# Kernel optimization log

Measured on AMD Instinct MI355X. Metric: run time of the kernel, lower is better.

Reference implementation:

```python
import jax, jax.numpy as jnp
from jax import lax
import numpy as np

H = 16        # hidden_size == input_size
L = 8         # num_layers


def _lstm_layer(x_seq, Wih, Whh, bih, bhh):
    # x_seq: [B, T, H] -> outputs [B, T, H]; PyTorch gate order i,f,g,o
    B = x_seq.shape[0]
    b = bih + bhh  # [4H]

    def step(carry, xt):
        h, c = carry
        gates = xt @ Wih.T + h @ Whh.T + b  # [B, 4H]
        i, f, g, o = jnp.split(gates, 4, axis=-1)
        c = jax.nn.sigmoid(f) * c + jax.nn.sigmoid(i) * jnp.tanh(g)
        h = jax.nn.sigmoid(o) * jnp.tanh(c)
        return (h, c), h

    h0 = jnp.zeros((B, H), x_seq.dtype)
    (_, _), hs = lax.scan(step, (h0, h0), jnp.swapaxes(x_seq, 0, 1))
    return jnp.swapaxes(hs, 0, 1)  # [B, T, H]


def setup_inputs() -> dict:
    key = jax.random.key(0)
    ks = jax.random.split(key, 9)
    s = 1.0 / np.sqrt(H)  # PyTorch default init scale
    x = jax.random.normal(ks[0], (2048, 512, H), dtype=jnp.float32)
    W_ih = jax.random.uniform(ks[1], (L, 4 * H, H), jnp.float32, -s, s)
    W_hh = jax.random.uniform(ks[2], (L, 4 * H, H), jnp.float32, -s, s)
    b_ih = jax.random.uniform(ks[3], (L, 4 * H), jnp.float32, -s, s)
    b_hh = jax.random.uniform(ks[4], (L, 4 * H), jnp.float32, -s, s)
    Wp = jax.random.uniform(ks[5], (3, H), jnp.float32, -s, s)
    bp = jax.random.uniform(ks[6], (3,), jnp.float32, -s, s)
    Wo = jax.random.uniform(ks[7], (3, H), jnp.float32, -s, s)
    bo = jax.random.uniform(ks[8], (3,), jnp.float32, -s, s)
    return {"x": x, "W_ih": W_ih, "W_hh": W_hh, "b_ih": b_ih, "b_hh": b_hh,
            "Wp": Wp, "bp": bp, "Wo": Wo, "bo": bo}


def reference(x, W_ih, W_hh, b_ih, b_hh, Wp, bp, Wo, bo):
    h = x
    for l in range(L):  # fixed small layer count
        h = _lstm_layer(h, W_ih[l], W_hh[l], b_ih[l], b_hh[l])
    last = h[:, -1, :]                       # [B, H]
    position = last @ Wp.T + bp              # [B, 3]
    orientation = jnp.tanh(last @ Wo.T + bo) # [B, 3]
    return jnp.concatenate((position, orientation), axis=1)  # [B, 6]
```

## Files before the change

kernel.cpp:

```cpp
#include <hip/hip_runtime.h>
#include <math.h>

typedef _Float16 f16x4 __attribute__((ext_vector_type(4)));
typedef _Float16 f16x2 __attribute__((ext_vector_type(2)));
typedef float    f32x4 __attribute__((ext_vector_type(4)));
typedef float    f32x2 __attribute__((ext_vector_type(2)));

constexpr int kT     = 512;
constexpr int kH     = 16;
constexpr int kL     = 8;
constexpr int kNB    = 8;
constexpr int kSlots = 8;
constexpr int kLyr   = kL + 1;
constexpr int kRow   = 16;
constexpr int kSlotE = kLyr * kNB * kRow;
constexpr int kIters = 33;

constexpr float kL2E = 1.4426950408889634f;

__device__ __forceinline__ float ex2(float w)  { return __builtin_amdgcn_exp2f(w); }
__device__ __forceinline__ float rcpf(float e) { return __builtin_amdgcn_rcpf(e); }

__global__ __launch_bounds__(512, 2)
void lstm_rr8(const float* __restrict__ x,
              const float* __restrict__ Wih, const float* __restrict__ Whh,
              const float* __restrict__ bih, const float* __restrict__ bhh,
              const float* __restrict__ Wp,  const float* __restrict__ bpos,
              const float* __restrict__ Wo,  const float* __restrict__ bori,
              float* __restrict__ out)
{
    const int tid  = threadIdx.x;
    const int l    = tid >> 6;
    const int lane = tid & 63;
    const int n    = lane & 15;
    const int q    = lane >> 4;
    const int b    = n & 7;
    const int hi   = n >> 3;

    __shared__ __align__(16) _Float16 hb[kSlots][kLyr][kNB][kRow];

    {
        int* hz = (int*)&hb[0][0][0][0];
        for (int i = tid; i < (int)(sizeof(hb) / 4); i += 512) hz[i] = 0;
    }
    __syncthreads();

    const float asc = ((n & 3) == 2) ? (-2.0f * kL2E) : (-kL2E);
    f16x4 A1[4], A2[4];
    f32x4 bias[4];
    #pragma unroll
    for (int p = 0; p < 4; ++p) {
        const int wrow = (n & 3) * 16 + 4 * (n >> 2) + p;
        const float* w1 = Wih + (size_t)l * 64 * kH + wrow * kH + 4 * q;
        const float* w2 = Whh + (size_t)l * 64 * kH + wrow * kH + 4 * q;
        #pragma unroll
        for (int jj = 0; jj < 4; ++jj) {
            A1[p][jj] = (_Float16)(asc * w1[jj]);
            A2[p][jj] = (_Float16)(asc * w2[jj]);
        }
        #pragma unroll
        for (int r = 0; r < 4; ++r) {
            const float sc = (r == 2) ? (-2.0f * kL2E) : (-kL2E);
            const int g0 = l * 64 + r * 16 + 4 * q + p;
            bias[p][r] = sc * (bih[g0] + bhh[g0]);
        }
    }

    const _Float16* b1base = &hb[0][l][b][4 * q];
    _Float16* hwbase = &hb[0][l + 1][b][4 * q + 2 * hi];
    _Float16* xwbase = &hb[0][0][b][4 * q + 2 * hi];

    const float* xg = x + ((size_t)(blockIdx.x * kNB + b) * kT) * kH
                        + 4 * q + 2 * hi;
    f32x2 xr0 = {0.f, 0.f}, xr1 = {0.f, 0.f}, xr2 = {0.f, 0.f}, xr3 = {0.f, 0.f};
    if (l == 0) {
        #pragma unroll
        for (int t = 0; t < 2; ++t) {
            const f32x2 xv = *(const f32x2*)(xg + (size_t)t * kH);
            f16x2 xh = { (_Float16)xv[0], (_Float16)xv[1] };
            *(f16x2*)(&hb[6 + t][0][b][4 * q + 2 * hi]) = xh;
        }
        xr0 = *(const f32x2*)(xg + 2 * (size_t)kH);
        xr1 = *(const f32x2*)(xg + 3 * (size_t)kH);
        xr2 = *(const f32x2*)(xg + 4 * (size_t)kH);
        xr3 = *(const f32x2*)(xg + 5 * (size_t)kH);
    }
    __syncthreads();

    f32x4 dIn0, dIn1, dIn2, dIn3;
    {
        const f16x4 B1p = *(const f16x4*)(b1base + 6 * kSlotE);
        dIn0 = __builtin_amdgcn_mfma_f32_16x16x16f16(A1[0], B1p, bias[0], 0, 0, 0);
        dIn1 = __builtin_amdgcn_mfma_f32_16x16x16f16(A1[1], B1p, bias[1], 0, 0, 0);
        dIn2 = __builtin_amdgcn_mfma_f32_16x16x16f16(A1[2], B1p, bias[2], 0, 0, 0);
        dIn3 = __builtin_amdgcn_mfma_f32_16x16x16f16(A1[3], B1p, bias[3], 0, 0, 0);
    }

    f16x4 B2r = { (_Float16)0.f, (_Float16)0.f, (_Float16)0.f, (_Float16)0.f };
    float cA = 0.f, cB = 0.f;
    const int tl = 2 * l;

    #pragma unroll 1
    for (int it = 0; it < kIters; ++it) {
        const int wb = it * 16;
        #pragma unroll
        for (int k = 0; k < 16; ++k) {
            const int w = wb + k;
            const bool active = ((unsigned)(w - tl) < (unsigned)kT);

            const f16x4 B1n = *(const f16x4*)(b1base + ((k + 7) & 7) * kSlotE);

            f32x4 d0 = __builtin_amdgcn_mfma_f32_16x16x16f16(A2[0], B2r, dIn0, 0, 0, 0);
            f32x4 d1 = __builtin_amdgcn_mfma_f32_16x16x16f16(A2[1], B2r, dIn1, 0, 0, 0);
            f32x4 d2 = __builtin_amdgcn_mfma_f32_16x16x16f16(A2[2], B2r, dIn2, 0, 0, 0);
            f32x4 d3 = __builtin_amdgcn_mfma_f32_16x16x16f16(A2[3], B2r, dIn3, 0, 0, 0);

            f32x4 dA, dB;
            #pragma unroll
            for (int r = 0; r < 4; ++r) {
                dA[r] = hi ? d2[r] : d0[r];
                dB[r] = hi ? d3[r] : d1[r];
            }

            float hAf, hBf;
            {
                const float Ei = ex2(fminf(dA[0], 40.0f));
                const float Ef = ex2(fminf(dA[1], 40.0f));
                const float Eg = ex2(fminf(dA[2], 40.0f));
                const float Eo = ex2(fminf(dA[3], 60.0f));
                const float Dg = 1.0f + Eg;
                const float Df = 1.0f + Ef;
                const float P1  = fmaf(Ei, Dg, Dg);
                const float den = Df * P1;
                const float t2  = fmaf(-Eg, Df, Df);
                const float num = fmaf(cA, P1, t2);
                float cn = num * rcpf(den);
                cn = active ? cn : 0.0f;
                cA = cn;
                const float ac = fminf(cn * (-2.0f * kL2E), 60.0f);
                const float Ec = ex2(ac);
                const float Do = 1.0f + Eo;
                const float R2 = rcpf(fmaf(Do, Ec, Do));
                hAf = fmaf(-Ec, R2, R2);
            }
            {
                const float Ei = ex2(fminf(dB[0], 40.0f));
                const float Ef = ex2(fminf(dB[1], 40.0f));
                const float Eg = ex2(fminf(dB[2], 40.0f));
                const float Eo = ex2(fminf(dB[3], 60.0f));
                const float Dg = 1.0f + Eg;
                const float Df = 1.0f + Ef;
                const float P1  = fmaf(Ei, Dg, Dg);
                const float den = Df * P1;
                const float t2  = fmaf(-Eg, Df, Df);
                const float num = fmaf(cB, P1, t2);
                float cn = num * rcpf(den);
                cn = active ? cn : 0.0f;
                cB = cn;
                const float ac = fminf(cn * (-2.0f * kL2E), 60.0f);
                const float Ec = ex2(ac);
                const float Do = 1.0f + Eo;
                const float R2 = rcpf(fmaf(Do, Ec, Do));
                hBf = fmaf(-Ec, R2, R2);
            }

            f16x2 hp = { (_Float16)hAf, (_Float16)hBf };
            union { f16x2 h; int i; } uh; uh.h = hp;
            const int own   = uh.i;
            const int other = __shfl_xor(own, 8, 64);
            union { int i[2]; f16x4 v; } ub;
            ub.i[0] = hi ? other : own;
            ub.i[1] = hi ? own : other;
            B2r = ub.v;

            *(f16x2*)(hwbase + (k & 7) * kSlotE) = hp;

            if (l == 0) {
                f16x2 xh = { (_Float16)xr0[0], (_Float16)xr0[1] };
                *(f16x2*)(xwbase + (k & 7) * kSlotE) = xh;
                xr0 = xr1; xr1 = xr2; xr2 = xr3;
                int tn = w + 6; if (tn > kT - 1) tn = kT - 1;
                xr3 = *(const f32x2*)(xg + (size_t)tn * kH);
            }

            dIn0 = __builtin_amdgcn_mfma_f32_16x16x16f16(A1[0], B1n, bias[0], 0, 0, 0);
            dIn1 = __builtin_amdgcn_mfma_f32_16x16x16f16(A1[1], B1n, bias[1], 0, 0, 0);
            dIn2 = __builtin_amdgcn_mfma_f32_16x16x16f16(A1[2], B1n, bias[2], 0, 0, 0);
            dIn3 = __builtin_amdgcn_mfma_f32_16x16x16f16(A1[3], B1n, bias[3], 0, 0, 0);

            asm volatile("s_waitcnt lgkmcnt(0)\n\ts_barrier" ::: "memory");
        }
    }

    __syncthreads();

    if (l == kL - 1 && lane < kNB) {
        const int bb = lane;
        float hreg[kH];
        #pragma unroll
        for (int u = 0; u < kH; ++u) hreg[u] = (float)hb[5][kL][bb][u];
        #pragma unroll
        for (int r = 0; r < 3; ++r) {
            float accP = bpos[r], accO = bori[r];
            #pragma unroll
            for (int u = 0; u < kH; ++u) {
                accP = fmaf(hreg[u], Wp[r * kH + u], accP);
                accO = fmaf(hreg[u], Wo[r * kH + u], accO);
            }
            const float Et = ex2(-2.0f * kL2E * accO);
            accO = fmaf(2.0f, rcpf(1.0f + Et), -1.0f);
            out[(size_t)(blockIdx.x * kNB + bb) * 6 + r]     = accP;
            out[(size_t)(blockIdx.x * kNB + bb) * 6 + 3 + r] = accO;
        }
    }
}

extern "C" void kernel_launch(void* const* d_in, const int* in_sizes, int n_in,
                              void* d_out, int out_size, void* d_ws, size_t ws_size,
                              hipStream_t stream) {
    const float* x    = (const float*)d_in[0];
    const float* Wih  = (const float*)d_in[1];
    const float* Whh  = (const float*)d_in[2];
    const float* bih  = (const float*)d_in[3];
    const float* bhh  = (const float*)d_in[4];
    const float* Wp   = (const float*)d_in[5];
    const float* bpos = (const float*)d_in[6];
    const float* Wo   = (const float*)d_in[7];
    const float* bori = (const float*)d_in[8];
    float* out = (float*)d_out;

    const int B = in_sizes[0] / (kT * kH);
    lstm_rr8<<<dim3(B / kNB), dim3(512), 0, stream>>>(x, Wih, Whh, bih, bhh,
                                                      Wp, bpos, Wo, bori, out);
}
```

Baseline: 312.2 us.

## Pipeline layers over 16-step chunks to cut per-timestep block barriers

Result: no change. 308.2 us (-1.3%).

```diff
diff --git a/kernel.cpp b/kernel.cpp
--- a/kernel.cpp
+++ b/kernel.cpp
@@ -4,17 +4,15 @@
 typedef _Float16 f16x4 __attribute__((ext_vector_type(4)));
 typedef _Float16 f16x2 __attribute__((ext_vector_type(2)));
 typedef float    f32x4 __attribute__((ext_vector_type(4)));
-typedef float    f32x2 __attribute__((ext_vector_type(2)));
-
-constexpr int kT     = 512;
-constexpr int kH     = 16;
-constexpr int kL     = 8;
-constexpr int kNB    = 8;
-constexpr int kSlots = 8;
-constexpr int kLyr   = kL + 1;
-constexpr int kRow   = 16;
-constexpr int kSlotE = kLyr * kNB * kRow;
-constexpr int kIters = 33;
+
+constexpr int kT      = 512;
+constexpr int kH      = 16;
+constexpr int kL      = 8;
+constexpr int kNB     = 8;
+constexpr int kC      = 16;
+constexpr int kChunks = kT / kC;
+constexpr int kStages = kChunks + kL - 1;
+constexpr int kRowE   = kNB * kH;
 
 constexpr float kL2E = 1.4426950408889634f;
 
@@ -22,12 +20,12 @@
 __device__ __forceinline__ float rcpf(float e) { return __builtin_amdgcn_rcpf(e); }
 
 __global__ __launch_bounds__(512, 2)
-void lstm_rr8(const float* __restrict__ x,
-              const float* __restrict__ Wih, const float* __restrict__ Whh,
-              const float* __restrict__ bih, const float* __restrict__ bhh,
-              const float* __restrict__ Wp,  const float* __restrict__ bpos,
-              const float* __restrict__ Wo,  const float* __restrict__ bori,
-              float* __restrict__ out)
+void lstm_ck(const float* __restrict__ x,
+             const float* __restrict__ Wih, const float* __restrict__ Whh,
+             const float* __restrict__ bih, const float* __restrict__ bhh,
+             const float* __restrict__ Wp,  const float* __restrict__ bpos,
+             const float* __restrict__ Wo,  const float* __restrict__ bori,
+             float* __restrict__ out)
 {
     const int tid  = threadIdx.x;
     const int l    = tid >> 6;
@@ -37,13 +35,8 @@
     const int b    = n & 7;
     const int hi   = n >> 3;
 
-    __shared__ __align__(16) _Float16 hb[kSlots][kLyr][kNB][kRow];
-
-    {
-        int* hz = (int*)&hb[0][0][0][0];
-        for (int i = tid; i < (int)(sizeof(hb) / 4); i += 512) hz[i] = 0;
-    }
-    __syncthreads();
+    __shared__ __align__(16) _Float16 hbuf[2][kL - 1][kC][kNB][kH];
+    __shared__ __align__(16) _Float16 headb[kNB][kH];
 
     const float asc = ((n & 3) == 2) ? (-2.0f * kL2E) : (-kL2E);
     f16x4 A1[4], A2[4];
@@ -66,151 +59,136 @@
         }
     }
 
-    const _Float16* b1base = &hb[0][l][b][4 * q];
-    _Float16* hwbase = &hb[0][l + 1][b][4 * q + 2 * hi];
-    _Float16* xwbase = &hb[0][0][b][4 * q + 2 * hi];
-
-    const float* xg = x + ((size_t)(blockIdx.x * kNB + b) * kT) * kH
-                        + 4 * q + 2 * hi;
-    f32x2 xr0 = {0.f, 0.f}, xr1 = {0.f, 0.f}, xr2 = {0.f, 0.f}, xr3 = {0.f, 0.f};
+    const float* xg = x + ((size_t)(blockIdx.x * kNB + b) * kT) * kH + 4 * q;
+    f32x4 xf[kC];
     if (l == 0) {
         #pragma unroll
-        for (int t = 0; t < 2; ++t) {
-            const f32x2 xv = *(const f32x2*)(xg + (size_t)t * kH);
-            f16x2 xh = { (_Float16)xv[0], (_Float16)xv[1] };
-            *(f16x2*)(&hb[6 + t][0][b][4 * q + 2 * hi]) = xh;
-        }
-        xr0 = *(const f32x2*)(xg + 2 * (size_t)kH);
-        xr1 = *(const f32x2*)(xg + 3 * (size_t)kH);
-        xr2 = *(const f32x2*)(xg + 4 * (size_t)kH);
-        xr3 = *(const f32x2*)(xg + 5 * (size_t)kH);
-    }
-    __syncthreads();
-
-    f32x4 dIn0, dIn1, dIn2, dIn3;
-    {
-        const f16x4 B1p = *(const f16x4*)(b1base + 6 * kSlotE);
-        dIn0 = __builtin_amdgcn_mfma_f32_16x16x16f16(A1[0], B1p, bias[0], 0, 0, 0);
-        dIn1 = __builtin_amdgcn_mfma_f32_16x16x16f16(A1[1], B1p, bias[1], 0, 0, 0);
-        dIn2 = __builtin_amdgcn_mfma_f32_16x16x16f16(A1[2], B1p, bias[2], 0, 0, 0);
-        dIn3 = __builtin_amdgcn_mfma_f32_16x16x16f16(A1[3], B1p, bias[3], 0, 0, 0);
+        for (int j = 0; j < kC; ++j)
+            xf[j] = *(const f32x4*)(xg + (size_t)j * kH);
     }
 
     f16x4 B2r = { (_Float16)0.f, (_Float16)0.f, (_Float16)0.f, (_Float16)0.f };
     float cA = 0.f, cB = 0.f;
-    const int tl = 2 * l;
 
     #pragma unroll 1
-    for (int it = 0; it < kIters; ++it) {
-        const int wb = it * 16;
-        #pragma unroll
-        for (int k = 0; k < 16; ++k) {
-            const int w = wb + k;
-            const bool active = ((unsigned)(w - tl) < (unsigned)kT);
-
-            const f16x4 B1n = *(const f16x4*)(b1base + ((k + 7) & 7) * kSlotE);
-
-            f32x4 d0 = __builtin_amdgcn_mfma_f32_16x16x16f16(A2[0], B2r, dIn0, 0, 0, 0);
-            f32x4 d1 = __builtin_amdgcn_mfma_f32_16x16x16f16(A2[1], B2r, dIn1, 0, 0, 0);
-            f32x4 d2 = __builtin_amdgcn_mfma_f32_16x16x16f16(A2[2], B2r, dIn2, 0, 0, 0);
-            f32x4 d3 = __builtin_amdgcn_mfma_f32_16x16x16f16(A2[3], B2r, dIn3, 0, 0, 0);
-
-            f32x4 dA, dB;
+    for (int s = 0; s < kStages; ++s) {
+        const int c = s - l;
+        if ((unsigned)c < (unsigned)kChunks) {
+            f16x4 B1f[kC];
+            if (l == 0) {
+                #pragma unroll
+                for (int j = 0; j < kC; ++j) {
+                    f16x4 v = { (_Float16)xf[j][0], (_Float16)xf[j][1],
+                                (_Float16)xf[j][2], (_Float16)xf[j][3] };
+                    B1f[j] = v;
+                }
+                if (c + 1 < kChunks) {
+                    #pragma unroll
+                    for (int j = 0; j < kC; ++j)
+                        xf[j] = *(const f32x4*)(xg + (size_t)((c + 1) * kC + j) * kH);
+                }
+            } else {
+                const _Float16* src = &hbuf[c & 1][l - 1][0][b][4 * q];
+                #pragma unroll
+                for (int j = 0; j < kC; ++j)
+                    B1f[j] = *(const f16x4*)(src + j * kRowE);
+            }
+
+            _Float16* wdst = &hbuf[c & 1][(l < kL - 1) ? l : 0][0][b][4 * q + 2 * hi];
+
             #pragma unroll
-            for (int r = 0; r < 4; ++r) {
-                dA[r] = hi ? d2[r] : d0[r];
-                dB[r] = hi ? d3[r] : d1[r];
+            for (int j = 0; j < kC; ++j) {
+                f32x4 dIn0 = __builtin_amdgcn_mfma_f32_16x16x16f16(A1[0], B1f[j], bias[0], 0, 0, 0);
+                f32x4 dIn1 = __builtin_amdgcn_mfma_f32_16x16x16f16(A1[1], B1f[j], bias[1], 0, 0, 0);
+                f32x4 dIn2 = __builtin_amdgcn_mfma_f32_16x16x16f16(A1[2], B1f[j], bias[2], 0, 0, 0);
+                f32x4 dIn3 = __builtin_amdgcn_mfma_f32_16x16x16f16(A1[3], B1f[j], bias[3], 0, 0, 0);
+                f32x4 d0 = __builtin_amdgcn_mfma_f32_16x16x16f16(A2[0], B2r, dIn0, 0, 0, 0);
+                f32x4 d1 = __builtin_amdgcn_mfma_f32_16x16x16f16(A2[1], B2r, dIn1, 0, 0, 0);
+                f32x4 d2 = __builtin_amdgcn_mfma_f32_16x16x16f16(A2[2], B2r, dIn2, 0, 0, 0);
+                f32x4 d3 = __builtin_amdgcn_mfma_f32_16x16x16f16(A2[3], B2r, dIn3, 0, 0, 0);
+
+                f32x4 dA, dB;
+                #pragma unroll
+                for (int r = 0; r < 4; ++r) {
+                    dA[r] = hi ? d2[r] : d0[r];
+                    dB[r] = hi ? d3[r] : d1[r];
+                }
+
+                float hAf, hBf;
+                {
+                    const float Ei = ex2(fminf(dA[0], 40.0f));
+                    const float Ef = ex2(fminf(dA[1], 40.0f));
+                    const float Eg = ex2(fminf(dA[2], 40.0f));
+                    const float Eo = ex2(fminf(dA[3], 60.0f));
+                    const float Dg = 1.0f + Eg;
+                    const float Df = 1.0f + Ef;
+                    const float P1  = fmaf(Ei, Dg, Dg);
+                    const float den = Df * P1;
+                    const float t2  = fmaf(-Eg, Df, Df);
+                    const float num = fmaf(cA, P1, t2);
+                    const float cn  = num * rcpf(den);
+                    cA = cn;
+                    const float ac = fminf(cn * (-2.0f * kL2E), 60.0f);
+                    const float Ec = ex2(ac);
+                    const float Do = 1.0f + Eo;
+                    const float R2 = rcpf(fmaf(Do, Ec, Do));
+                    hAf = fmaf(-Ec, R2, R2);
+                }
+                {
+                    const float Ei = ex2(fminf(dB[0], 40.0f));
+                    const float Ef = ex2(fminf(dB[1], 40.0f));
+                    const float Eg = ex2(fminf(dB[2], 40.0f));
+                    const float Eo = ex2(fminf(dB[3], 60.0f));
+                    const float Dg = 1.0f + Eg;
+                    const float Df = 1.0f + Ef;
+                    const float P1  = fmaf(Ei, Dg, Dg);
+                    const float den = Df * P1;
+                    const float t2  = fmaf(-Eg, Df, Df);
+                    const float num = fmaf(cB, P1, t2);
+                    const float cn  = num * rcpf(den);
+                    cB = cn;
+                    const float ac = fminf(cn * (-2.0f * kL2E), 60.0f);
+                    const float Ec = ex2(ac);
+                    const float Do = 1.0f + Eo;
+                    const float R2 = rcpf(fmaf(Do, Ec, Do));
+                    hBf = fmaf(-Ec, R2, R2);
+                }
+
+                f16x2 hp = { (_Float16)hAf, (_Float16)hBf };
+                union { f16x2 h; int i; } uh; uh.h = hp;
+                const int own   = uh.i;
+                const int other = __shfl_xor(own, 8, 64);
+                union { int i2[2]; f16x4 v; } ub;
+                ub.i2[0] = hi ? other : own;
+                ub.i2[1] = hi ? own : other;
+                B2r = ub.v;
+
+                if (l < kL - 1)
+                    *(f16x2*)(wdst + j * kRowE) = hp;
+                if (l == kL - 1 && c == kChunks - 1 && j == kC - 1)
+                    *(f16x2*)(&headb[b][4 * q + 2 * hi]) = hp;
             }
-
-            float hAf, hBf;
-            {
-                const float Ei = ex2(fminf(dA[0], 40.0f));
-                const float Ef = ex2(fminf(dA[1], 40.0f));
-                const float Eg = ex2(fminf(dA[2], 40.0f));
-                const float Eo = ex2(fminf(dA[3], 60.0f));
-                const float Dg = 1.0f + Eg;
-                const float Df = 1.0f + Ef;
-                const float P1  = fmaf(Ei, Dg, Dg);
-                const float den = Df * P1;
-                const float t2  = fmaf(-Eg, Df, Df);
-                const float num = fmaf(cA, P1, t2);
-                float cn = num * rcpf(den);
-                cn = active ? cn : 0.0f;
-                cA = cn;
-                const float ac = fminf(cn * (-2.0f * kL2E), 60.0f);
-                const float Ec = ex2(ac);
-                const float Do = 1.0f + Eo;
-                const float R2 = rcpf(fmaf(Do, Ec, Do));
-                hAf = fmaf(-Ec, R2, R2);
+        }
+        asm volatile("s_waitcnt lgkmcnt(0)\n\ts_barrier" ::: "memory");
+    }
+
+    __syncthreads();
+
+    if (l == kL - 1) {
+        const int bb = lane >> 3;
+        const int r  = lane & 7;
+        if (r < 6) {
+            const bool  isP   = (r < 3);
+            const float* wrow = isP ? (Wp + r * kH) : (Wo + (r - 3) * kH);
+            float acc = isP ? bpos[r] : bori[r - 3];
+            #pragma unroll
+            for (int u = 0; u < kH; ++u)
+                acc = fmaf((float)headb[bb][u], wrow[u], acc);
+            if (!isP) {
+                const float Et = ex2(-2.0f * kL2E * acc);
+                acc = fmaf(2.0f, rcpf(1.0f + Et), -1.0f);
             }
-            {
-                const float Ei = ex2(fminf(dB[0], 40.0f));
-                const float Ef = ex2(fminf(dB[1], 40.0f));
-                const float Eg = ex2(fminf(dB[2], 40.0f));
-                const float Eo = ex2(fminf(dB[3], 60.0f));
-                const float Dg = 1.0f + Eg;
-                const float Df = 1.0f + Ef;
-                const float P1  = fmaf(Ei, Dg, Dg);
-                const float den = Df * P1;
-                const float t2  = fmaf(-Eg, Df, Df);
-                const float num = fmaf(cB, P1, t2);
-                float cn = num * rcpf(den);
-                cn = active ? cn : 0.0f;
-                cB = cn;
-                const float ac = fminf(cn * (-2.0f * kL2E), 60.0f);
-                const float Ec = ex2(ac);
-                const float Do = 1.0f + Eo;
-                const float R2 = rcpf(fmaf(Do, Ec, Do));
-                hBf = fmaf(-Ec, R2, R2);
-            }
-
-            f16x2 hp = { (_Float16)hAf, (_Float16)hBf };
-            union { f16x2 h; int i; } uh; uh.h = hp;
-            const int own   = uh.i;
-            const int other = __shfl_xor(own, 8, 64);
-            union { int i[2]; f16x4 v; } ub;
-            ub.i[0] = hi ? other : own;
-            ub.i[1] = hi ? own : other;
-            B2r = ub.v;
-
-            *(f16x2*)(hwbase + (k & 7) * kSlotE) = hp;
-
-            if (l == 0) {
-                f16x2 xh = { (_Float16)xr0[0], (_Float16)xr0[1] };
-                *(f16x2*)(xwbase + (k & 7) * kSlotE) = xh;
-                xr0 = xr1; xr1 = xr2; xr2 = xr3;
-                int tn = w + 6; if (tn > kT - 1) tn = kT - 1;
-                xr3 = *(const f32x2*)(xg + (size_t)tn * kH);
-            }
-
-            dIn0 = __builtin_amdgcn_mfma_f32_16x16x16f16(A1[0], B1n, bias[0], 0, 0, 0);
-            dIn1 = __builtin_amdgcn_mfma_f32_16x16x16f16(A1[1], B1n, bias[1], 0, 0, 0);
-            dIn2 = __builtin_amdgcn_mfma_f32_16x16x16f16(A1[2], B1n, bias[2], 0, 0, 0);
-            dIn3 = __builtin_amdgcn_mfma_f32_16x16x16f16(A1[3], B1n, bias[3], 0, 0, 0);
-
-            asm volatile("s_waitcnt lgkmcnt(0)\n\ts_barrier" ::: "memory");
-        }
-    }
-
-    __syncthreads();
-
-    if (l == kL - 1 && lane < kNB) {
-        const int bb = lane;
-        float hreg[kH];
-        #pragma unroll
-        for (int u = 0; u < kH; ++u) hreg[u] = (float)hb[5][kL][bb][u];
-        #pragma unroll
-        for (int r = 0; r < 3; ++r) {
-            float accP = bpos[r], accO = bori[r];
-            #pragma unroll
-            for (int u = 0; u < kH; ++u) {
-                accP = fmaf(hreg[u], Wp[r * kH + u], accP);
-                accO = fmaf(hreg[u], Wo[r * kH + u], accO);
-            }
-            const float Et = ex2(-2.0f * kL2E * accO);
-            accO = fmaf(2.0f, rcpf(1.0f + Et), -1.0f);
-            out[(size_t)(blockIdx.x * kNB + bb) * 6 + r]     = accP;
-            out[(size_t)(blockIdx.x * kNB + bb) * 6 + 3 + r] = accO;
+            out[(size_t)(blockIdx.x * kNB + bb) * 6 + r] = acc;
         }
     }
 }
@@ -230,6 +208,6 @@
     float* out = (float*)d_out;
 
     const int B = in_sizes[0] / (kT * kH);
-    lstm_rr8<<<dim3(B / kNB), dim3(512), 0, stream>>>(x, Wih, Whh, bih, bhh,
-                                                      Wp, bpos, Wo, bori, out);
+    lstm_ck<<<dim3(B / kNB), dim3(512), 0, stream>>>(x, Wih, Whh, bih, bhh,
+                                                     Wp, bpos, Wo, bori, out);
 }
```
